# Optimization experiments

Hardware: AMD Instinct MI355X
Metric: run time of the kernel (lower is better)

Reference implementation:

```python
import jax, jax.numpy as jnp
import numpy as np

LN_EPS = 1e-5

def setup_inputs() -> dict:
    key = jax.random.key(0)
    ks = jax.random.split(key, 12)
    B, S, M, C, D = 16, 1024, 4096, 768, 256
    inp = {
        'seed_xyz_norm': jax.random.normal(ks[0], (B, S, 3), jnp.float32),
        'p_last': jax.random.normal(ks[1], (B, M, 3), jnp.float32),
        'f_last': jax.random.normal(ks[2], (B, C, M), jnp.float32),
        'seed_features': jax.random.normal(ks[3], (B, D, S), jnp.float32),
        # LayerNorm params over C
        'ln_gamma': jnp.ones((C,), jnp.float32),
        'ln_beta': jnp.zeros((C,), jnp.float32),
        # conv1d projector C -> 256 (kernel size 1) + ReLU
        'proj_w': jax.random.normal(ks[4], (D, C), jnp.float32) * (1.0 / np.sqrt(C)),
        'proj_b': jnp.zeros((D,), jnp.float32),
        # fusion MLP: concat512 -> 512 -> 256 (1x1 convs)
        'mlp_w1': jax.random.normal(ks[5], (2 * D, 2 * D), jnp.float32) * (1.0 / np.sqrt(2 * D)),
        'mlp_b1': jnp.zeros((2 * D,), jnp.float32),
        'mlp_w2': jax.random.normal(ks[6], (D, 2 * D), jnp.float32) * (1.0 / np.sqrt(2 * D)),
        'mlp_b2': jnp.zeros((D,), jnp.float32),
    }
    return inp


def reference(seed_xyz_norm, p_last, f_last, seed_features,
              ln_gamma, ln_beta, proj_w, proj_b,
              mlp_w1, mlp_b1, mlp_w2, mlp_b2):
    # --- nearest_neighbor_gather_features ---
    # squared distance [B,S,M]; argmin over M, gather features [B,C,S]
    d2 = jnp.sum(seed_xyz_norm * seed_xyz_norm, -1, keepdims=True) \
         - 2.0 * jnp.einsum('bsd,bmd->bsm', seed_xyz_norm, p_last) \
         + jnp.sum(p_last * p_last, -1)[:, None, :]
    idx = jnp.argmin(d2, axis=-1)                                   # [B,S]
    lift3d_raw = jnp.take_along_axis(f_last, idx[:, None, :], axis=2)  # [B,C,S]

    # --- LayerNorm over channel dim C ---
    mu = jnp.mean(lift3d_raw, axis=1, keepdims=True)
    var = jnp.mean((lift3d_raw - mu) ** 2, axis=1, keepdims=True)
    x_ln = (lift3d_raw - mu) * jax.lax.rsqrt(var + LN_EPS)
    x_ln = x_ln * ln_gamma[None, :, None] + ln_beta[None, :, None]

    # --- conv1d projector (1x1) + ReLU ---
    proj = jax.nn.relu(jnp.einsum('oc,bcs->bos', proj_w, x_ln) + proj_b[None, :, None])

    # --- concat fusion MLP ---
    fused = jnp.concatenate([seed_features, proj], axis=1)          # [B,512,S]
    h = jax.nn.relu(jnp.einsum('oc,bcs->bos', mlp_w1, fused) + mlp_b1[None, :, None])
    mixed = jnp.einsum('oc,bcs->bos', mlp_w2, h) + mlp_b2[None, :, None]  # [B,256,S]
    return mixed
```

## Files before the change

### kernel.cpp

```cpp
#include <hip/hip_runtime.h>

namespace {

constexpr int B = 16, S = 1024, M = 4096, C = 768, D = 256;

typedef __attribute__((ext_vector_type(8))) short bf16x8;
typedef __attribute__((ext_vector_type(4))) float f32x4;

__device__ inline ushort f2bf(float f) {
  uint u = __float_as_uint(f);
  uint r = (u + 0x7FFFu + ((u >> 16) & 1u)) >> 16;
  return (ushort)r;
}

__global__ __launch_bounds__(256)
void nn_kernel(const float* __restrict__ xyz, const float* __restrict__ p,
               int* __restrict__ idx_out) {
  const int b = blockIdx.y;
  const int t = threadIdx.x;
  const int seed = blockIdx.x * 16 + (t >> 4);
  const int l16 = t & 15;

  const float sx = xyz[((size_t)b * S + seed) * 3 + 0];
  const float sy = xyz[((size_t)b * S + seed) * 3 + 1];
  const float sz = xyz[((size_t)b * S + seed) * 3 + 2];
  const float ss = __fadd_rn(__fadd_rn(__fmul_rn(sx, sx), __fmul_rn(sy, sy)),
                             __fmul_rn(sz, sz));

  __shared__ float4 pt[256];

  float best = 3.4028235e38f;
  int besti = 0;
  const float* pb = p + (size_t)b * M * 3;

  for (int m0 = 0; m0 < M; m0 += 256) {
    __syncthreads();
    {
      const float a0 = pb[(size_t)(m0 + t) * 3 + 0];
      const float a1 = pb[(size_t)(m0 + t) * 3 + 1];
      const float a2 = pb[(size_t)(m0 + t) * 3 + 2];
      const float pp = __fadd_rn(__fadd_rn(__fmul_rn(a0, a0), __fmul_rn(a1, a1)),
                                 __fmul_rn(a2, a2));
      pt[t] = make_float4(a0, a1, a2, pp);
    }
    __syncthreads();
    #pragma unroll 4
    for (int j = l16; j < 256; j += 16) {
      const float4 q = pt[j];
      float dot = __fmul_rn(sx, q.x);
      dot = __fadd_rn(dot, __fmul_rn(sy, q.y));
      dot = __fadd_rn(dot, __fmul_rn(sz, q.z));
      const float d2 = __fadd_rn(__fsub_rn(ss, __fmul_rn(2.0f, dot)), q.w);
      const int mi = m0 + j;
      if (d2 < best || (d2 == best && mi < besti)) { best = d2; besti = mi; }
    }
  }
  #pragma unroll
  for (int off = 8; off >= 1; off >>= 1) {
    const float ob = __shfl_xor(best, off, 16);
    const int   oi = __shfl_xor(besti, off, 16);
    if (ob < best || (ob == best && oi < besti)) { best = ob; besti = oi; }
  }
  if (l16 == 0) idx_out[b * S + seed] = besti;
}

__global__ __launch_bounds__(256)
void bucket_sort_kernel(const int* __restrict__ idx, int* __restrict__ sIdx,
                        int* __restrict__ sS) {
  const int b = blockIdx.x;
  const int t = threadIdx.x;
  __shared__ int keys[1024];
  __shared__ int cnt[256];
  __shared__ int base[256];
  __shared__ int wsum[4];

  cnt[t] = 0;
  #pragma unroll
  for (int i = 0; i < 4; ++i) keys[t + 256 * i] = idx[b * S + t + 256 * i];
  __syncthreads();
  #pragma unroll
  for (int i = 0; i < 4; ++i) atomicAdd(&cnt[keys[t + 256 * i] >> 4], 1);
  __syncthreads();

  const int v = cnt[t];
  int sc = v;
  #pragma unroll
  for (int off = 1; off < 64; off <<= 1) {
    const int o = __shfl_up(sc, off);
    if ((t & 63) >= off) sc += o;
  }
  if ((t & 63) == 63) wsum[t >> 6] = sc;
  __syncthreads();
  int wb = 0;
  #pragma unroll
  for (int w = 0; w < 4; ++w)
    if (w < (t >> 6)) wb += wsum[w];
  base[t] = wb + sc - v;
  cnt[t] = 0;
  __syncthreads();

  #pragma unroll
  for (int i = 0; i < 4; ++i) {
    const int s = t + 256 * i;
    const int m = keys[s];
    const int bu = m >> 4;
    const int r = base[bu] + atomicAdd(&cnt[bu], 1);
    sIdx[b * S + r] = m;
    sS[b * S + r] = s;
  }
}

__global__ __launch_bounds__(256)
void gather_ln_kernel(const float* __restrict__ f, const int* __restrict__ sIdx,
                      const int* __restrict__ sS,
                      const float* __restrict__ gamma, const float* __restrict__ beta,
                      ushort* __restrict__ xln) {
  const int b = blockIdx.y;
  const int rl = blockIdx.x;
  const int r0 = (((rl & 7) << 6) + (rl >> 3)) << 1;
  const int t = threadIdx.x;
  const int sA = sS[b * S + r0],     mA = sIdx[b * S + r0];
  const int sB = sS[b * S + r0 + 1], mB = sIdx[b * S + r0 + 1];

  const float* fb = f + (size_t)b * C * M;
  const float a0 = fb[(size_t)(t      ) * M + mA];
  const float a1 = fb[(size_t)(t + 256) * M + mA];
  const float a2 = fb[(size_t)(t + 512) * M + mA];
  const float c0 = fb[(size_t)(t      ) * M + mB];
  const float c1 = fb[(size_t)(t + 256) * M + mB];
  const float c2 = fb[(size_t)(t + 512) * M + mB];

  const float g0 = gamma[t], g1 = gamma[t + 256], g2 = gamma[t + 512];
  const float e0 = beta[t],  e1 = beta[t + 256],  e2 = beta[t + 512];

  __shared__ float redA[4], redB[4], stats[4];
  const int wave = t >> 6;

  float psA = a0 + a1 + a2;
  float psB = c0 + c1 + c2;
  #pragma unroll
  for (int off = 32; off >= 1; off >>= 1) {
    psA += __shfl_xor(psA, off);
    psB += __shfl_xor(psB, off);
  }
  if ((t & 63) == 0) { redA[wave] = psA; redB[wave] = psB; }
  __syncthreads();
  if (t == 0) {
    stats[0] = (redA[0] + redA[1] + redA[2] + redA[3]) * (1.0f / 768.0f);
    stats[1] = (redB[0] + redB[1] + redB[2] + redB[3]) * (1.0f / 768.0f);
  }
  __syncthreads();
  const float muA = stats[0], muB = stats[1];

  const float dA0 = a0 - muA, dA1 = a1 - muA, dA2 = a2 - muA;
  const float dB0 = c0 - muB, dB1 = c1 - muB, dB2 = c2 - muB;
  float pvA = dA0 * dA0 + dA1 * dA1 + dA2 * dA2;
  float pvB = dB0 * dB0 + dB1 * dB1 + dB2 * dB2;
  #pragma unroll
  for (int off = 32; off >= 1; off >>= 1) {
    pvA += __shfl_xor(pvA, off);
    pvB += __shfl_xor(pvB, off);
  }
  if ((t & 63) == 0) { redA[wave] = pvA; redB[wave] = pvB; }
  __syncthreads();
  if (t == 0) {
    const float varA = (redA[0] + redA[1] + redA[2] + redA[3]) * (1.0f / 768.0f);
    const float varB = (redB[0] + redB[1] + redB[2] + redB[3]) * (1.0f / 768.0f);
    stats[2] = 1.0f / sqrtf(varA + 1e-5f);
    stats[3] = 1.0f / sqrtf(varB + 1e-5f);
  }
  __syncthreads();
  const float rsA = stats[2], rsB = stats[3];

  ushort* oA = xln + ((size_t)b * S + sA) * C;
  ushort* oB = xln + ((size_t)b * S + sB) * C;
  oA[t      ] = f2bf((dA0 * rsA) * g0 + e0);
  oA[t + 256] = f2bf((dA1 * rsA) * g1 + e1);
  oA[t + 512] = f2bf((dA2 * rsA) * g2 + e2);
  oB[t      ] = f2bf((dB0 * rsB) * g0 + e0);
  oB[t + 256] = f2bf((dB1 * rsB) * g1 + e1);
  oB[t + 512] = f2bf((dB2 * rsB) * g2 + e2);
}

__global__ __launch_bounds__(256)
void transpose_sf_kernel(const float* __restrict__ sf, ushort* __restrict__ fused) {
  const int b = blockIdx.z;
  const int d0 = blockIdx.y * 64;
  const int s0 = blockIdx.x * 64;
  const int t = threadIdx.x;
  __shared__ float tile[64][68];

  const float* inb = sf + ((size_t)b * D + d0) * S + s0;
  #pragma unroll
  for (int q = 0; q < 4; ++q) {
    const int rr = (t >> 4) + q * 16;
    const int c4 = (t & 15) * 4;
    const float4 v = *(const float4*)&inb[(size_t)rr * S + c4];
    *(float4*)&tile[rr][c4] = v;
  }
  __syncthreads();
  #pragma unroll
  for (int q = 0; q < 4; ++q) {
    const int srow = (t >> 4) + q * 16;
    const int dc = (t & 15) * 4;
    ushort4 o;
    o.x = f2bf(tile[dc + 0][srow]);
    o.y = f2bf(tile[dc + 1][srow]);
    o.z = f2bf(tile[dc + 2][srow]);
    o.w = f2bf(tile[dc + 3][srow]);
    *(ushort4*)&fused[((size_t)b * S + s0 + srow) * 512 + d0 + dc] = o;
  }
}

__global__ __launch_bounds__(256)
void convert_w_kernel(const float* __restrict__ w0, int n0, ushort* __restrict__ o0,
                      const float* __restrict__ w1, int n1, ushort* __restrict__ o1,
                      const float* __restrict__ w2, int n2, ushort* __restrict__ o2) {
  const int which = blockIdx.y;
  const float* src = which == 0 ? w0 : which == 1 ? w1 : w2;
  ushort* dst = which == 0 ? o0 : which == 1 ? o1 : o2;
  const int n = which == 0 ? n0 : which == 1 ? n1 : n2;
  const int i = (blockIdx.x * 256 + threadIdx.x) * 4;
  if (i < n) {
    const float4 v = *(const float4*)&src[i];
    ushort4 o;
    o.x = f2bf(v.x); o.y = f2bf(v.y); o.z = f2bf(v.z); o.w = f2bf(v.w);
    *(ushort4*)&dst[i] = o;
  }
}

__global__ __launch_bounds__(256)
void gemm_bf16_kernel(const ushort* __restrict__ W, int K, int O,
                      const ushort* __restrict__ X,
                      const float* __restrict__ bias,
                      void* __restrict__ out, int outMode, int ldOut, int colOff,
                      int relu) {
  const int b  = blockIdx.z;
  const int s0 = blockIdx.x * 128;
  const int o0 = blockIdx.y * 128;
  const int t  = threadIdx.x;
  const int wave = t >> 6;
  const int lane = t & 63;
  const int l16 = lane & 15;
  const int quad = lane >> 4;

  __shared__ ushort Wt[128 * 40];
  __shared__ ushort Xt[128 * 40];
  __shared__ float biasS[128];

  if (t < 128) biasS[t] = bias[o0 + t];

  f32x4 acc[8][2];
  const f32x4 z = {0.f, 0.f, 0.f, 0.f};
  #pragma unroll
  for (int of = 0; of < 8; ++of) { acc[of][0] = z; acc[of][1] = z; }

  const ushort* Xb = X + (size_t)b * S * K;
  const int kg = t & 3;
  const int row = t >> 2;
  const size_t wBase = (size_t)(o0 + row) * K + kg * 8;
  const size_t xBase = (size_t)(s0 + row) * K + kg * 8;
  const size_t wBase2 = wBase + (size_t)64 * K;
  const size_t xBase2 = xBase + (size_t)64 * K;

  uint4 wv0 = *(const uint4*)&W[wBase];
  uint4 wv1 = *(const uint4*)&W[wBase2];
  uint4 xv0 = *(const uint4*)&Xb[xBase];
  uint4 xv1 = *(const uint4*)&Xb[xBase2];

  for (int c0 = 0; c0 < K; c0 += 32) {
    __syncthreads();
    *(uint4*)&Wt[row * 40 + kg * 8] = wv0;
    *(uint4*)&Wt[(row + 64) * 40 + kg * 8] = wv1;
    *(uint4*)&Xt[row * 40 + kg * 8] = xv0;
    *(uint4*)&Xt[(row + 64) * 40 + kg * 8] = xv1;
    __syncthreads();

    if (c0 + 32 < K) {
      wv0 = *(const uint4*)&W[wBase + c0 + 32];
      wv1 = *(const uint4*)&W[wBase2 + c0 + 32];
      xv0 = *(const uint4*)&Xb[xBase + c0 + 32];
      xv1 = *(const uint4*)&Xb[xBase2 + c0 + 32];
    }

    bf16x8 bfr[2];
    #pragma unroll
    for (int sf = 0; sf < 2; ++sf)
      bfr[sf] = *(const bf16x8*)&Xt[(wave * 32 + sf * 16 + l16) * 40 + quad * 8];
    #pragma unroll
    for (int of = 0; of < 8; ++of) {
      const bf16x8 afr = *(const bf16x8*)&Wt[(of * 16 + l16) * 40 + quad * 8];
      acc[of][0] = __builtin_amdgcn_mfma_f32_16x16x32_bf16(afr, bfr[0], acc[of][0], 0, 0, 0);
      acc[of][1] = __builtin_amdgcn_mfma_f32_16x16x32_bf16(afr, bfr[1], acc[of][1], 0, 0, 0);
    }
  }

  if (outMode == 0) {
    ushort* ob = (ushort*)out;
    #pragma unroll
    for (int of = 0; of < 8; ++of) {
      #pragma unroll
      for (int sf = 0; sf < 2; ++sf) {
        const int s = s0 + wave * 32 + sf * 16 + l16;
        const int ol = of * 16 + quad * 4;
        float v0 = acc[of][sf].x + biasS[ol + 0];
        float v1 = acc[of][sf].y + biasS[ol + 1];
        float v2 = acc[of][sf].z + biasS[ol + 2];
        float v3 = acc[of][sf].w + biasS[ol + 3];
        if (relu) {
          v0 = fmaxf(v0, 0.f); v1 = fmaxf(v1, 0.f);
          v2 = fmaxf(v2, 0.f); v3 = fmaxf(v3, 0.f);
        }
        ushort4 st;
        st.x = f2bf(v0); st.y = f2bf(v1); st.z = f2bf(v2); st.w = f2bf(v3);
        *(ushort4*)&ob[((size_t)b * S + s) * ldOut + colOff + o0 + ol] = st;
      }
    }
  } else {
    float* o32 = (float*)out;
    #pragma unroll
    for (int of = 0; of < 8; ++of) {
      #pragma unroll
      for (int sf = 0; sf < 2; ++sf) {
        const int s = s0 + wave * 32 + sf * 16 + l16;
        const int ol = of * 16 + quad * 4;
        const float vr[4] = {acc[of][sf].x, acc[of][sf].y, acc[of][sf].z, acc[of][sf].w};
        #pragma unroll
        for (int r = 0; r < 4; ++r) {
          const int o = o0 + ol + r;
          o32[((size_t)b * O + o) * S + s] = vr[r] + biasS[ol + r];
        }
      }
    }
  }
}

}

extern "C" void kernel_launch(void* const* d_in, const int* in_sizes, int n_in,
                              void* d_out, int out_size, void* d_ws, size_t ws_size,
                              hipStream_t stream) {
  const float* seed_xyz  = (const float*)d_in[0];
  const float* p_last    = (const float*)d_in[1];
  const float* f_last    = (const float*)d_in[2];
  const float* seed_feat = (const float*)d_in[3];
  const float* ln_gamma  = (const float*)d_in[4];
  const float* ln_beta   = (const float*)d_in[5];
  const float* proj_w    = (const float*)d_in[6];
  const float* proj_b    = (const float*)d_in[7];
  const float* mlp_w1    = (const float*)d_in[8];
  const float* mlp_b1    = (const float*)d_in[9];
  const float* mlp_w2    = (const float*)d_in[10];
  const float* mlp_b2    = (const float*)d_in[11];
  float* out = (float*)d_out;

  char* ws = (char*)d_ws;
  int*    idx   = (int*)(ws);
  int*    sIdx  = (int*)(ws + (64 << 10));
  int*    sS    = (int*)(ws + (128 << 10));
  ushort* wp_bf = (ushort*)(ws + (256 << 10));
  ushort* w1_bf = (ushort*)(ws + (640 << 10));
  ushort* w2_bf = (ushort*)(ws + (1152 << 10));
  ushort* xln   = (ushort*)(ws + (2ull << 20));
  ushort* fused = (ushort*)(ws + (26ull << 20));
  ushort* hbuf  = (ushort*)(ws + (42ull << 20));

  nn_kernel<<<dim3(S / 16, B), 256, 0, stream>>>(seed_xyz, p_last, idx);
  bucket_sort_kernel<<<dim3(B), 256, 0, stream>>>(idx, sIdx, sS);

  gather_ln_kernel<<<dim3(S / 2, B), 256, 0, stream>>>(f_last, sIdx, sS,
                                                       ln_gamma, ln_beta, xln);

  transpose_sf_kernel<<<dim3(S / 64, D / 64, B), 256, 0, stream>>>(seed_feat, fused);
  convert_w_kernel<<<dim3(256, 3), 256, 0, stream>>>(
      proj_w, D * C, wp_bf, mlp_w1, 512 * 512, w1_bf, mlp_w2, 256 * 512, w2_bf);

  gemm_bf16_kernel<<<dim3(S / 128, 256 / 128, B), 256, 0, stream>>>(
      wp_bf, C, 256, xln, proj_b, fused, 0, 512, 256, 1);

  gemm_bf16_kernel<<<dim3(S / 128, 512 / 128, B), 256, 0, stream>>>(
      w1_bf, 512, 512, fused, mlp_b1, hbuf, 0, 512, 0, 1);

  gemm_bf16_kernel<<<dim3(S / 128, 256 / 128, B), 256, 0, stream>>>(
      w2_bf, 512, 256, hbuf, mlp_b2, out, 1, 0, 0, 0);
}
```

Measured before the change: 410.0 us.

## Batch four rows per gather-LN block, merge prep kernels, double-buffer GEMM LDS

The gather+LayerNorm kernel now handles four sorted seeds per block instead of two. This halves the number of blocks and increases the independent strided loads in flight per thread. The transpose and weight-conversion kernels are merged into one launch to save a kernel launch. The bf16 MFMA GEMM gains double-buffered shared memory tiles with a two-deep register prefetch, cutting one barrier per K step at the cost of twice the LDS use and more registers.

Measured after the change: 409.1 us. No clear change (-0.2%).

```diff
diff --git a/kernel.cpp b/kernel.cpp
--- a/kernel.cpp
+++ b/kernel.cpp
@@ -117,115 +117,132 @@
                       ushort* __restrict__ xln) {
   const int b = blockIdx.y;
   const int rl = blockIdx.x;
-  const int r0 = (((rl & 7) << 6) + (rl >> 3)) << 1;
+  const int r0 = (((rl & 7) << 5) + (rl >> 3)) << 2;
   const int t = threadIdx.x;
-  const int sA = sS[b * S + r0],     mA = sIdx[b * S + r0];
-  const int sB = sS[b * S + r0 + 1], mB = sIdx[b * S + r0 + 1];
+
+  int sR[4], mR[4];
+  #pragma unroll
+  for (int i = 0; i < 4; ++i) {
+    sR[i] = sS[b * S + r0 + i];
+    mR[i] = sIdx[b * S + r0 + i];
+  }
 
   const float* fb = f + (size_t)b * C * M;
-  const float a0 = fb[(size_t)(t      ) * M + mA];
-  const float a1 = fb[(size_t)(t + 256) * M + mA];
-  const float a2 = fb[(size_t)(t + 512) * M + mA];
-  const float c0 = fb[(size_t)(t      ) * M + mB];
-  const float c1 = fb[(size_t)(t + 256) * M + mB];
-  const float c2 = fb[(size_t)(t + 512) * M + mB];
+  float v[4][3];
+  #pragma unroll
+  for (int i = 0; i < 4; ++i) {
+    v[i][0] = fb[(size_t)(t      ) * M + mR[i]];
+    v[i][1] = fb[(size_t)(t + 256) * M + mR[i]];
+    v[i][2] = fb[(size_t)(t + 512) * M + mR[i]];
+  }
 
   const float g0 = gamma[t], g1 = gamma[t + 256], g2 = gamma[t + 512];
   const float e0 = beta[t],  e1 = beta[t + 256],  e2 = beta[t + 512];
 
-  __shared__ float redA[4], redB[4], stats[4];
+  __shared__ float red[4][4];
+  __shared__ float stats[8];
   const int wave = t >> 6;
 
-  float psA = a0 + a1 + a2;
-  float psB = c0 + c1 + c2;
+  float ps[4];
+  #pragma unroll
+  for (int i = 0; i < 4; ++i) ps[i] = v[i][0] + v[i][1] + v[i][2];
   #pragma unroll
   for (int off = 32; off >= 1; off >>= 1) {
-    psA += __shfl_xor(psA, off);
-    psB += __shfl_xor(psB, off);
-  }
-  if ((t & 63) == 0) { redA[wave] = psA; redB[wave] = psB; }
-  __syncthreads();
-  if (t == 0) {
-    stats[0] = (redA[0] + redA[1] + redA[2] + redA[3]) * (1.0f / 768.0f);
-    stats[1] = (redB[0] + redB[1] + redB[2] + redB[3]) * (1.0f / 768.0f);
-  }
-  __syncthreads();
-  const float muA = stats[0], muB = stats[1];
-
-  const float dA0 = a0 - muA, dA1 = a1 - muA, dA2 = a2 - muA;
-  const float dB0 = c0 - muB, dB1 = c1 - muB, dB2 = c2 - muB;
-  float pvA = dA0 * dA0 + dA1 * dA1 + dA2 * dA2;
-  float pvB = dB0 * dB0 + dB1 * dB1 + dB2 * dB2;
+    #pragma unroll
+    for (int i = 0; i < 4; ++i) ps[i] += __shfl_xor(ps[i], off);
+  }
+  if ((t & 63) == 0) {
+    #pragma unroll
+    for (int i = 0; i < 4; ++i) red[i][wave] = ps[i];
+  }
+  __syncthreads();
+  if (t < 4)
+    stats[t] = (red[t][0] + red[t][1] + red[t][2] + red[t][3]) * (1.0f / 768.0f);
+  __syncthreads();
+
+  float d[4][3];
+  #pragma unroll
+  for (int i = 0; i < 4; ++i) {
+    const float mu = stats[i];
+    d[i][0] = v[i][0] - mu; d[i][1] = v[i][1] - mu; d[i][2] = v[i][2] - mu;
+  }
+  float pv[4];
+  #pragma unroll
+  for (int i = 0; i < 4; ++i)
+    pv[i] = d[i][0] * d[i][0] + d[i][1] * d[i][1] + d[i][2] * d[i][2];
   #pragma unroll
   for (int off = 32; off >= 1; off >>= 1) {
-    pvA += __shfl_xor(pvA, off);
-    pvB += __shfl_xor(pvB, off);
-  }
-  if ((t & 63) == 0) { redA[wave] = pvA; redB[wave] = pvB; }
-  __syncthreads();
-  if (t == 0) {
-    const float varA = (redA[0] + redA[1] + redA[2] + redA[3]) * (1.0f / 768.0f);
-    const float varB = (redB[0] + redB[1] + redB[2] + redB[3]) * (1.0f / 768.0f);
-    stats[2] = 1.0f / sqrtf(varA + 1e-5f);
-    stats[3] = 1.0f / sqrtf(varB + 1e-5f);
-  }
-  __syncthreads();
-  const float rsA = stats[2], rsB = stats[3];
-
-  ushort* oA = xln + ((size_t)b * S + sA) * C;
-  ushort* oB = xln + ((size_t)b * S + sB) * C;
-  oA[t      ] = f2bf((dA0 * rsA) * g0 + e0);
-  oA[t + 256] = f2bf((dA1 * rsA) * g1 + e1);
-  oA[t + 512] = f2bf((dA2 * rsA) * g2 + e2);
-  oB[t      ] = f2bf((dB0 * rsB) * g0 + e0);
-  oB[t + 256] = f2bf((dB1 * rsB) * g1 + e1);
-  oB[t + 512] = f2bf((dB2 * rsB) * g2 + e2);
+    #pragma unroll
+    for (int i = 0; i < 4; ++i) pv[i] += __shfl_xor(pv[i], off);
+  }
+  if ((t & 63) == 0) {
+    #pragma unroll
+    for (int i = 0; i < 4; ++i) red[i][wave] = pv[i];
+  }
+  __syncthreads();
+  if (t < 4) {
+    const float var = (red[t][0] + red[t][1] + red[t][2] + red[t][3]) * (1.0f / 768.0f);
+    stats[4 + t] = 1.0f / sqrtf(var + 1e-5f);
+  }
+  __syncthreads();
+
+  #pragma unroll
+  for (int i = 0; i < 4; ++i) {
+    const float rs = stats[4 + i];
+    ushort* o = xln + ((size_t)b * S + sR[i]) * C;
+    o[t      ] = f2bf((d[i][0] * rs) * g0 + e0);
+    o[t + 256] = f2bf((d[i][1] * rs) * g1 + e1);
+    o[t + 512] = f2bf((d[i][2] * rs) * g2 + e2);
+  }
 }
 
 __global__ __launch_bounds__(256)
-void transpose_sf_kernel(const float* __restrict__ sf, ushort* __restrict__ fused) {
-  const int b = blockIdx.z;
-  const int d0 = blockIdx.y * 64;
-  const int s0 = blockIdx.x * 64;
+void prep_kernel(const float* __restrict__ sf, ushort* __restrict__ fused,
+                 const float* __restrict__ w0, int n0, ushort* __restrict__ o0,
+                 const float* __restrict__ w1, int n1, ushort* __restrict__ o1,
+                 const float* __restrict__ w2, int n2, ushort* __restrict__ o2) {
+  __shared__ float tile[64][68];
+  const int bid = blockIdx.x;
   const int t = threadIdx.x;
-  __shared__ float tile[64][68];
-
-  const float* inb = sf + ((size_t)b * D + d0) * S + s0;
-  #pragma unroll
-  for (int q = 0; q < 4; ++q) {
-    const int rr = (t >> 4) + q * 16;
-    const int c4 = (t & 15) * 4;
-    const float4 v = *(const float4*)&inb[(size_t)rr * S + c4];
-    *(float4*)&tile[rr][c4] = v;
-  }
-  __syncthreads();
-  #pragma unroll
-  for (int q = 0; q < 4; ++q) {
-    const int srow = (t >> 4) + q * 16;
-    const int dc = (t & 15) * 4;
-    ushort4 o;
-    o.x = f2bf(tile[dc + 0][srow]);
-    o.y = f2bf(tile[dc + 1][srow]);
-    o.z = f2bf(tile[dc + 2][srow]);
-    o.w = f2bf(tile[dc + 3][srow]);
-    *(ushort4*)&fused[((size_t)b * S + s0 + srow) * 512 + d0 + dc] = o;
-  }
-}
-
-__global__ __launch_bounds__(256)
-void convert_w_kernel(const float* __restrict__ w0, int n0, ushort* __restrict__ o0,
-                      const float* __restrict__ w1, int n1, ushort* __restrict__ o1,
-                      const float* __restrict__ w2, int n2, ushort* __restrict__ o2) {
-  const int which = blockIdx.y;
-  const float* src = which == 0 ? w0 : which == 1 ? w1 : w2;
-  ushort* dst = which == 0 ? o0 : which == 1 ? o1 : o2;
-  const int n = which == 0 ? n0 : which == 1 ? n1 : n2;
-  const int i = (blockIdx.x * 256 + threadIdx.x) * 4;
-  if (i < n) {
-    const float4 v = *(const float4*)&src[i];
-    ushort4 o;
-    o.x = f2bf(v.x); o.y = f2bf(v.y); o.z = f2bf(v.z); o.w = f2bf(v.w);
-    *(ushort4*)&dst[i] = o;
+
+  if (bid < 1024) {
+    const int b  = bid >> 6;
+    const int d0 = ((bid >> 4) & 3) * 64;
+    const int s0 = (bid & 15) * 64;
+
+    const float* inb = sf + ((size_t)b * D + d0) * S + s0;
+    #pragma unroll
+    for (int q = 0; q < 4; ++q) {
+      const int rr = (t >> 4) + q * 16;
+      const int c4 = (t & 15) * 4;
+      const float4 v = *(const float4*)&inb[(size_t)rr * S + c4];
+      *(float4*)&tile[rr][c4] = v;
+    }
+    __syncthreads();
+    #pragma unroll
+    for (int q = 0; q < 4; ++q) {
+      const int srow = (t >> 4) + q * 16;
+      const int dc = (t & 15) * 4;
+      ushort4 o;
+      o.x = f2bf(tile[dc + 0][srow]);
+      o.y = f2bf(tile[dc + 1][srow]);
+      o.z = f2bf(tile[dc + 2][srow]);
+      o.w = f2bf(tile[dc + 3][srow]);
+      *(ushort4*)&fused[((size_t)b * S + s0 + srow) * 512 + d0 + dc] = o;
+    }
+  } else {
+    const int id = bid - 1024;
+    const int which = id >> 8;
+    const float* src = which == 0 ? w0 : which == 1 ? w1 : w2;
+    ushort* dst = which == 0 ? o0 : which == 1 ? o1 : o2;
+    const int n = which == 0 ? n0 : which == 1 ? n1 : n2;
+    const int i = ((id & 255) * 256 + t) * 4;
+    if (i < n) {
+      const float4 v = *(const float4*)&src[i];
+      ushort4 o;
+      o.x = f2bf(v.x); o.y = f2bf(v.y); o.z = f2bf(v.z); o.w = f2bf(v.w);
+      *(ushort4*)&dst[i] = o;
+    }
   }
 }
 
@@ -244,8 +261,8 @@
   const int l16 = lane & 15;
   const int quad = lane >> 4;
 
-  __shared__ ushort Wt[128 * 40];
-  __shared__ ushort Xt[128 * 40];
+  __shared__ ushort Wt[2][128 * 40];
+  __shared__ ushort Xt[2][128 * 40];
   __shared__ float biasS[128];
 
   if (t < 128) biasS[t] = bias[o0 + t];
@@ -262,37 +279,51 @@
   const size_t xBase = (size_t)(s0 + row) * K + kg * 8;
   const size_t wBase2 = wBase + (size_t)64 * K;
   const size_t xBase2 = xBase + (size_t)64 * K;
+  const int T = K >> 5;
 
   uint4 wv0 = *(const uint4*)&W[wBase];
   uint4 wv1 = *(const uint4*)&W[wBase2];
   uint4 xv0 = *(const uint4*)&Xb[xBase];
   uint4 xv1 = *(const uint4*)&Xb[xBase2];
-
-  for (int c0 = 0; c0 < K; c0 += 32) {
-    __syncthreads();
-    *(uint4*)&Wt[row * 40 + kg * 8] = wv0;
-    *(uint4*)&Wt[(row + 64) * 40 + kg * 8] = wv1;
-    *(uint4*)&Xt[row * 40 + kg * 8] = xv0;
-    *(uint4*)&Xt[(row + 64) * 40 + kg * 8] = xv1;
-    __syncthreads();
-
-    if (c0 + 32 < K) {
-      wv0 = *(const uint4*)&W[wBase + c0 + 32];
-      wv1 = *(const uint4*)&W[wBase2 + c0 + 32];
-      xv0 = *(const uint4*)&Xb[xBase + c0 + 32];
-      xv1 = *(const uint4*)&Xb[xBase2 + c0 + 32];
-    }
-
+  *(uint4*)&Wt[0][row * 40 + kg * 8] = wv0;
+  *(uint4*)&Wt[0][(row + 64) * 40 + kg * 8] = wv1;
+  *(uint4*)&Xt[0][row * 40 + kg * 8] = xv0;
+  *(uint4*)&Xt[0][(row + 64) * 40 + kg * 8] = xv1;
+  if (T > 1) {
+    wv0 = *(const uint4*)&W[wBase + 32];
+    wv1 = *(const uint4*)&W[wBase2 + 32];
+    xv0 = *(const uint4*)&Xb[xBase + 32];
+    xv1 = *(const uint4*)&Xb[xBase2 + 32];
+  }
+  __syncthreads();
+
+  for (int tt = 0; tt < T; ++tt) {
+    const int cur = tt & 1;
+
+    if (tt + 1 < T) {
+      *(uint4*)&Wt[cur ^ 1][row * 40 + kg * 8] = wv0;
+      *(uint4*)&Wt[cur ^ 1][(row + 64) * 40 + kg * 8] = wv1;
+      *(uint4*)&Xt[cur ^ 1][row * 40 + kg * 8] = xv0;
+      *(uint4*)&Xt[cur ^ 1][(row + 64) * 40 + kg * 8] = xv1;
+    }
+    if (tt + 2 < T) {
+      const int c = (tt + 2) * 32;
+      wv0 = *(const uint4*)&W[wBase + c];
+      wv1 = *(const uint4*)&W[wBase2 + c];
+      xv0 = *(const uint4*)&Xb[xBase + c];
+      xv1 = *(const uint4*)&Xb[xBase2 + c];
+    }
     bf16x8 bfr[2];
     #pragma unroll
     for (int sf = 0; sf < 2; ++sf)
-      bfr[sf] = *(const bf16x8*)&Xt[(wave * 32 + sf * 16 + l16) * 40 + quad * 8];
+      bfr[sf] = *(const bf16x8*)&Xt[cur][(wave * 32 + sf * 16 + l16) * 40 + quad * 8];
     #pragma unroll
     for (int of = 0; of < 8; ++of) {
-      const bf16x8 afr = *(const bf16x8*)&Wt[(of * 16 + l16) * 40 + quad * 8];
+      const bf16x8 afr = *(const bf16x8*)&Wt[cur][(of * 16 + l16) * 40 + quad * 8];
       acc[of][0] = __builtin_amdgcn_mfma_f32_16x16x32_bf16(afr, bfr[0], acc[of][0], 0, 0, 0);
       acc[of][1] = __builtin_amdgcn_mfma_f32_16x16x32_bf16(afr, bfr[1], acc[of][1], 0, 0, 0);
     }
+    __syncthreads();
   }
 
   if (outMode == 0) {
@@ -368,11 +399,11 @@
   nn_kernel<<<dim3(S / 16, B), 256, 0, stream>>>(seed_xyz, p_last, idx);
   bucket_sort_kernel<<<dim3(B), 256, 0, stream>>>(idx, sIdx, sS);
 
-  gather_ln_kernel<<<dim3(S / 2, B), 256, 0, stream>>>(f_last, sIdx, sS,
+  gather_ln_kernel<<<dim3(S / 4, B), 256, 0, stream>>>(f_last, sIdx, sS,
                                                        ln_gamma, ln_beta, xln);
 
-  transpose_sf_kernel<<<dim3(S / 64, D / 64, B), 256, 0, stream>>>(seed_feat, fused);
-  convert_w_kernel<<<dim3(256, 3), 256, 0, stream>>>(
+  prep_kernel<<<dim3(1024 + 768), 256, 0, stream>>>(
+      seed_feat, fused,
       proj_w, D * C, wp_bf, mlp_w1, 512 * 512, w1_bf, mlp_w2, 256 * 512, w2_bf);
 
   gemm_bf16_kernel<<<dim3(S / 128, 256 / 128, B), 256, 0, stream>>>(
```
